# Optimization experiments

Hardware: AMD Instinct MI355X
Metric: run time of the kernel (lower is better)

Reference implementation:

```python
import jax, jax.numpy as jnp
import numpy as np

H_SPLITS = [2, 3, 3]          # crpe_window {3:2, 5:3, 7:3}
K_SIZES = [3, 5, 7]
NUM_HEADS = 8
EPS = 1e-6


def dwconv(x, w, b, k):
    # x: (B,C,H,W), w: (C,1,k,k) depthwise, 'same' padding
    y = jax.lax.conv_general_dilated(
        x, w, (1, 1), [(k // 2, k // 2)] * 2,
        feature_group_count=x.shape[1],
        dimension_numbers=('NCHW', 'OIHW', 'NCHW'))
    return y + b[None, :, None, None]


def layernorm(x, g, b):
    m = jnp.mean(x, -1, keepdims=True)
    v = jnp.var(x, -1, keepdims=True)
    return (x - m) * jax.lax.rsqrt(v + EPS) * g + b


def conv_rel_pos_enc(q, v, ws, bs, H, W):
    # ConvRelPosEnc (MPViT style, no cls token): q * depthwise_conv(v)
    B, h, N, Ch = q.shape
    v_img = v.transpose(0, 1, 3, 2).reshape(B, h * Ch, H, W)  # B (h Ch) H W
    splits = np.cumsum([hs * Ch for hs in H_SPLITS])[:-1]
    parts = jnp.split(v_img, splits, axis=1)
    conv_v = jnp.concatenate(
        [dwconv(p, w, b, k) for p, w, b, k in zip(parts, ws, bs, K_SIZES)], axis=1)
    conv_v = conv_v.reshape(B, h, Ch, N).transpose(0, 1, 3, 2)
    return q * conv_v


def setup_inputs() -> dict:
    key = jax.random.key(0)
    B, H, W, C, nd, r, mr = 8, 64, 64, 320, 4, 2, 4
    h = NUM_HEADS
    N = H * W
    Ch = C // h
    hid = C // r
    ks = jax.random.split(key, 16)
    s = 0.02
    return {
        'x': jax.random.normal(ks[0], (B, N, C), jnp.float32),
        'domain_label': jax.nn.one_hot(jax.random.randint(ks[1], (B,), 0, nd), nd, dtype=jnp.float32),
        'cpe_w': jax.random.normal(ks[2], (C, 1, 3, 3), jnp.float32) * s,
        'cpe_b': jnp.zeros((C,), jnp.float32),
        'ln1_g': jnp.ones((C,), jnp.float32), 'ln1_b': jnp.zeros((C,), jnp.float32),
        'qkv_w': jax.random.normal(ks[3], (3 * C, C), jnp.float32) * s,
        'qkv_b': jnp.zeros((3 * C,), jnp.float32),
        'crpe_w3': jax.random.normal(ks[4], (2 * Ch, 1, 3, 3), jnp.float32) * s,
        'crpe_b3': jnp.zeros((2 * Ch,), jnp.float32),
        'crpe_w5': jax.random.normal(ks[5], (3 * Ch, 1, 5, 5), jnp.float32) * s,
        'crpe_b5': jnp.zeros((3 * Ch,), jnp.float32),
        'crpe_w7': jax.random.normal(ks[6], (3 * Ch, 1, 7, 7), jnp.float32) * s,
        'crpe_b7': jnp.zeros((3 * Ch,), jnp.float32),
        'dom_w1': jax.random.normal(ks[7], (hid, nd), jnp.float32) * s,
        'dom_b1': jnp.zeros((hid,), jnp.float32),
        'dom_w2': jax.random.normal(ks[8], (C, hid), jnp.float32) * s,
        'dom_b2': jnp.zeros((C,), jnp.float32),
        'proj_w': jax.random.normal(ks[9], (C, C), jnp.float32) * s,
        'proj_b': jnp.zeros((C,), jnp.float32),
        'ln2_g': jnp.ones((C,), jnp.float32), 'ln2_b': jnp.zeros((C,), jnp.float32),
        'mlp_w1': jax.random.normal(ks[10], (mr * C, C), jnp.float32) * s,
        'mlp_b1': jnp.zeros((mr * C,), jnp.float32),
        'mlp_w2': jax.random.normal(ks[11], (C, mr * C), jnp.float32) * s,
        'mlp_b2': jnp.zeros((C,), jnp.float32),
        'H': H, 'W': W,
    }


def reference(x, domain_label, cpe_w, cpe_b, ln1_g, ln1_b, qkv_w, qkv_b,
              crpe_w3, crpe_b3, crpe_w5, crpe_b5, crpe_w7, crpe_b7,
              dom_w1, dom_b1, dom_w2, dom_b2, proj_w, proj_b,
              ln2_g, ln2_b, mlp_w1, mlp_b1, mlp_w2, mlp_b2, H, W):
    B, N, C = x.shape
    h = NUM_HEADS
    Ch = C // h
    scale = Ch ** -0.5
    # ConvPosEnc: depthwise 3x3 conv + residual
    img = x.transpose(0, 2, 1).reshape(B, C, H, W)
    x = (dwconv(img, cpe_w, cpe_b, 3) + img).reshape(B, C, N).transpose(0, 2, 1)
    # FactorAtt_ConvRelPosEnc_Sup
    cur = layernorm(x, ln1_g, ln1_b)
    qkv = (cur @ qkv_w.T + qkv_b).reshape(B, N, 3, h, Ch).transpose(2, 0, 3, 1, 4)
    q, k, v = qkv[0], qkv[1], qkv[2]          # (B,h,N,Ch) each
    k_sm = jax.nn.softmax(k, axis=2)          # softmax over tokens
    kv = jnp.einsum('bhnk,bhnv->bhkv', k_sm, v)   # (B,h,Ch,Ch)
    fa = jnp.einsum('bhnk,bhkv->bhnv', q, kv)
    fa = scale * fa + conv_rel_pos_enc(
        q, v, (crpe_w3, crpe_w5, crpe_w7), (crpe_b3, crpe_b5, crpe_b7), H, W)
    # domain gate: MLP(one_hot) -> softmax over heads, broadcast over tokens
    d = jax.nn.relu(domain_label @ dom_w1.T + dom_b1) @ dom_w2.T + dom_b2  # (B,C)
    d = jax.nn.softmax(d.reshape(B, h, 1, Ch), axis=1)
    att = (d * fa).transpose(0, 2, 1, 3).reshape(B, N, C)
    x = x + (att @ proj_w.T + proj_b)
    # MLP (GELU, ratio 4)
    cur = layernorm(x, ln2_g, ln2_b)
    cur = jax.nn.gelu(cur @ mlp_w1.T + mlp_b1, approximate=False) @ mlp_w2.T + mlp_b2
    return x + cur
```

## Files before the change

### kernel.cpp

```cpp
#include <hip/hip_runtime.h>
#include <hip/hip_bf16.h>
#include <math.h>
#include <type_traits>

#define B_    8
#define Nn    4096
#define Cc    320
#define QS    1024
#define ATT_SCALE 0.15811388300841897f

typedef __attribute__((ext_vector_type(8))) short s8v;
typedef __attribute__((ext_vector_type(4))) float f4v;

__device__ __forceinline__ float bf2f(short u) {
    return __uint_as_float(((unsigned int)(unsigned short)u) << 16);
}
__device__ __forceinline__ short f2bf(float f) {
    return (short)__bfloat16_as_ushort(__float2bfloat16(f));
}
__device__ __forceinline__ float gelu_fast(float v) {
    float u = v * (0.7978845608f + 0.0356774081f * v * v);
    float e = __expf(2.f * u);
    float t = 1.f - 2.f / (e + 1.f);
    return 0.5f * v * (1.f + t);
}

typedef const __attribute__((address_space(1))) unsigned int* gp1_t;
typedef __attribute__((address_space(3))) unsigned int* lp3_t;
__device__ __forceinline__ void gload16(const void* g, void* l) {
    __builtin_amdgcn_global_load_lds((gp1_t)g, (lp3_t)l, 16, 0, 0);
}

__global__ void cvt_all(const float* __restrict__ s0, const float* __restrict__ s1,
                        const float* __restrict__ s2, const float* __restrict__ s3,
                        __hip_bfloat16* __restrict__ d) {
    int i = blockIdx.x * 256 + threadIdx.x;
    if (i >= 1351680) return;
    const float* s; int j, rows, K;
    if (i < 327680)      { s = s0; j = i;          rows = 960;  K = 320; }
    else if (i < 450560) { s = s1; j = i - 327680; rows = 320;  K = 320; }
    else if (i < 860160) { s = s2; j = i - 450560; rows = 1280; K = 320; }
    else                 { s = s3; j = i - 860160; rows = 320;  K = 1280; }
    float v = (j / K < rows) ? s[j] : 0.f;
    d[i] = __float2bfloat16(v);
}

template<typename T>
__global__ void ln_kernel(const T* __restrict__ x, const float* __restrict__ g,
                          const float* __restrict__ bt, __hip_bfloat16* __restrict__ out) {
    int bn = blockIdx.x;
    int lane = threadIdx.x;
    const T* row = x + (size_t)bn * Cc;
    float v[5];
    float s = 0.f, s2 = 0.f;
    #pragma unroll
    for (int i = 0; i < 5; ++i) {
        if constexpr (std::is_same<T, float>::value) v[i] = row[lane + 64 * i];
        else v[i] = bf2f(((const short*)row)[lane + 64 * i]);
        s += v[i];
        s2 += v[i] * v[i];
    }
    #pragma unroll
    for (int off = 32; off > 0; off >>= 1) {
        s  += __shfl_down(s, off);
        s2 += __shfl_down(s2, off);
    }
    s  = __shfl(s, 0);
    s2 = __shfl(s2, 0);
    float mean = s * (1.f / 320.f);
    float var  = s2 * (1.f / 320.f) - mean * mean;
    float rstd = rsqrtf(var + 1e-6f);
    __hip_bfloat16* orow = out + (size_t)bn * Cc;
    #pragma unroll
    for (int i = 0; i < 5; ++i) {
        int c = lane + 64 * i;
        orow[c] = __float2bfloat16((v[i] - mean) * rstd * g[c] + bt[c]);
    }
}

template<int ACT, int RES, int WF32, int WBF16, int KT>
__global__ __launch_bounds__(512) void gemm_mfma(
        const __hip_bfloat16* __restrict__ A, const __hip_bfloat16* __restrict__ W,
        const float* __restrict__ bias, const void* __restrict__ resv,
        float* __restrict__ outf, __hip_bfloat16* __restrict__ outb,
        int NS, int Nreal, int gy) {
    __shared__ __align__(16) short As[256 * 64];
    __shared__ __align__(16) short Bs[128 * 64];
    int bid = blockIdx.x;
    int grp8 = gy << 3;
    int grp = bid / grp8, rem = bid % grp8;
    int m0 = ((grp << 3) + (rem & 7)) << 8;
    int n0 = (rem >> 3) << 7;
    int tid = threadIdx.x;
    int w = tid >> 6, lane = tid & 63;
    int wr = w >> 1, wc = w & 1;
    int lrow = lane & 15, lk = lane >> 4;
    f4v acc[4][4];
    #pragma unroll
    for (int i = 0; i < 4; ++i)
        #pragma unroll
        for (int j = 0; j < 4; ++j) acc[i][j] = (f4v){0.f, 0.f, 0.f, 0.f};

    int srow = (w << 3) + (lane >> 3);
    int slot = lane & 7;

    #pragma unroll
    for (int k0 = 0; k0 < KT; k0 += 64) {
        __syncthreads();
        #pragma unroll
        for (int i = 0; i < 4; ++i) {
            int row = i * 64 + srow;
            int sk = (slot ^ (row & 7)) << 3;
            gload16(&A[(size_t)(m0 + row) * KT + k0 + sk], &As[i * 4096 + w * 512]);
        }
        #pragma unroll
        for (int i = 0; i < 2; ++i) {
            int row = i * 64 + srow;
            int sk = (slot ^ (row & 7)) << 3;
            gload16(&W[(size_t)(n0 + row) * KT + k0 + sk], &Bs[i * 4096 + w * 512]);
        }
        __syncthreads();
        #pragma unroll
        for (int ks = 0; ks < 2; ++ks) {
            s8v af[4], bf[4];
            #pragma unroll
            for (int mi = 0; mi < 4; ++mi) {
                int row = wr * 64 + mi * 16 + lrow;
                int s = (ks * 4 + lk) ^ (row & 7);
                af[mi] = *reinterpret_cast<const s8v*>(&As[row * 64 + s * 8]);
            }
            #pragma unroll
            for (int ni = 0; ni < 4; ++ni) {
                int row = wc * 64 + ni * 16 + lrow;
                int s = (ks * 4 + lk) ^ (row & 7);
                bf[ni] = *reinterpret_cast<const s8v*>(&Bs[row * 64 + s * 8]);
            }
            #pragma unroll
            for (int mi = 0; mi < 4; ++mi)
                #pragma unroll
                for (int ni = 0; ni < 4; ++ni)
                    acc[mi][ni] = __builtin_amdgcn_mfma_f32_16x16x32_bf16(bf[ni], af[mi], acc[mi][ni], 0, 0, 0);
        }
    }
    #pragma unroll
    for (int mi = 0; mi < 4; ++mi) {
        int m = m0 + wr * 64 + mi * 16 + lrow;
        #pragma unroll
        for (int ni = 0; ni < 4; ++ni) {
            int n = n0 + wc * 64 + ni * 16 + (lk << 2);
            if (n >= Nreal) continue;
            f4v v4 = acc[mi][ni];
            float4 bv = *reinterpret_cast<const float4*>(&bias[n]);
            v4[0] += bv.x; v4[1] += bv.y; v4[2] += bv.z; v4[3] += bv.w;
            if (RES == 1) {
                const float* res = (const float*)resv;
                float4 rv = *reinterpret_cast<const float4*>(&res[(size_t)m * NS + n]);
                v4[0] += rv.x; v4[1] += rv.y; v4[2] += rv.z; v4[3] += rv.w;
            } else if (RES == 2) {
                const short* res = (const short*)resv;
                short4 rv = *reinterpret_cast<const short4*>(&res[(size_t)m * NS + n]);
                v4[0] += bf2f(rv.x); v4[1] += bf2f(rv.y);
                v4[2] += bf2f(rv.z); v4[3] += bf2f(rv.w);
            }
            if (ACT == 1) {
                #pragma unroll
                for (int r = 0; r < 4; ++r) v4[r] = gelu_fast(v4[r]);
            }
            if (WF32)
                *reinterpret_cast<float4*>(&outf[(size_t)m * NS + n]) =
                    make_float4(v4[0], v4[1], v4[2], v4[3]);
            if (WBF16) {
                ushort4 u;
                u.x = (unsigned short)f2bf(v4[0]);
                u.y = (unsigned short)f2bf(v4[1]);
                u.z = (unsigned short)f2bf(v4[2]);
                u.w = (unsigned short)f2bf(v4[3]);
                *reinterpret_cast<ushort4*>(&outb[(size_t)m * NS + n]) = u;
            }
        }
    }
}

template<int ACT, int RES, int WF32, int WBF16, int KT, int LN>
__global__ __launch_bounds__(512) void gemm_fulln(
        const __hip_bfloat16* __restrict__ A, const __hip_bfloat16* __restrict__ W,
        const float* __restrict__ bias, const void* __restrict__ resv,
        float* __restrict__ outf, __hip_bfloat16* __restrict__ outb, int NS,
        const float* __restrict__ lng, const float* __restrict__ lnb,
        __hip_bfloat16* __restrict__ lnout) {
    __shared__ __align__(16) short As[64 * 64];
    __shared__ __align__(16) short Ws[320 * 64];
    int tid = threadIdx.x;
    int m0 = blockIdx.x << 6;
    int w = tid >> 6, lane = tid & 63;
    int wr = w >> 2, wc = w & 3;
    int lrow = lane & 15, lk = lane >> 4;
    f4v acc[2][5];
    #pragma unroll
    for (int i = 0; i < 2; ++i)
        #pragma unroll
        for (int j = 0; j < 5; ++j) acc[i][j] = (f4v){0.f, 0.f, 0.f, 0.f};

    int srow = tid >> 3;
    int slot = tid & 7;

    #pragma unroll
    for (int k0 = 0; k0 < KT; k0 += 64) {
        __syncthreads();
        {
            int sk = (slot ^ (srow & 7)) << 3;
            gload16(&A[(size_t)(m0 + srow) * KT + k0 + sk], &As[w * 512]);
        }
        #pragma unroll
        for (int i = 0; i < 5; ++i) {
            int row = i * 64 + srow;
            int sk = (slot ^ (row & 7)) << 3;
            gload16(&W[(size_t)row * KT + k0 + sk], &Ws[i * 4096 + w * 512]);
        }
        __syncthreads();
        #pragma unroll
        for (int ks = 0; ks < 2; ++ks) {
            s8v af[2], bf[5];
            #pragma unroll
            for (int mi = 0; mi < 2; ++mi) {
                int row = wr * 32 + mi * 16 + lrow;
                int s = (ks * 4 + lk) ^ (row & 7);
                af[mi] = *reinterpret_cast<const s8v*>(&As[row * 64 + s * 8]);
            }
            #pragma unroll
            for (int ni = 0; ni < 5; ++ni) {
                int row = wc * 80 + ni * 16 + lrow;
                int s = (ks * 4 + lk) ^ (row & 7);
                bf[ni] = *reinterpret_cast<const s8v*>(&Ws[row * 64 + s * 8]);
            }
            #pragma unroll
            for (int mi = 0; mi < 2; ++mi)
                #pragma unroll
                for (int ni = 0; ni < 5; ++ni)
                    acc[mi][ni] = __builtin_amdgcn_mfma_f32_16x16x32_bf16(bf[ni], af[mi], acc[mi][ni], 0, 0, 0);
        }
    }
    float psum[2] = {0.f, 0.f}, psq[2] = {0.f, 0.f};
    #pragma unroll
    for (int mi = 0; mi < 2; ++mi) {
        int m = m0 + wr * 32 + mi * 16 + lrow;
        #pragma unroll
        for (int ni = 0; ni < 5; ++ni) {
            int n = wc * 80 + ni * 16 + (lk << 2);
            f4v v4 = acc[mi][ni];
            float4 bv = *reinterpret_cast<const float4*>(&bias[n]);
            v4[0] += bv.x; v4[1] += bv.y; v4[2] += bv.z; v4[3] += bv.w;
            if (RES == 1) {
                const float* res = (const float*)resv;
                float4 rv = *reinterpret_cast<const float4*>(&res[(size_t)m * NS + n]);
                v4[0] += rv.x; v4[1] += rv.y; v4[2] += rv.z; v4[3] += rv.w;
            } else if (RES == 2) {
                const short* res = (const short*)resv;
                short4 rv = *reinterpret_cast<const short4*>(&res[(size_t)m * NS + n]);
                v4[0] += bf2f(rv.x); v4[1] += bf2f(rv.y);
                v4[2] += bf2f(rv.z); v4[3] += bf2f(rv.w);
            }
            if (ACT == 1) {
                #pragma unroll
                for (int r = 0; r < 4; ++r) v4[r] = gelu_fast(v4[r]);
            }
            if (WF32)
                *reinterpret_cast<float4*>(&outf[(size_t)m * NS + n]) =
                    make_float4(v4[0], v4[1], v4[2], v4[3]);
            if (WBF16) {
                ushort4 u;
                u.x = (unsigned short)f2bf(v4[0]);
                u.y = (unsigned short)f2bf(v4[1]);
                u.z = (unsigned short)f2bf(v4[2]);
                u.w = (unsigned short)f2bf(v4[3]);
                *reinterpret_cast<ushort4*>(&outb[(size_t)m * NS + n]) = u;
            }
            if (LN) {
                acc[mi][ni] = v4;
                psum[mi] += v4[0] + v4[1] + v4[2] + v4[3];
                psq[mi]  += v4[0]*v4[0] + v4[1]*v4[1] + v4[2]*v4[2] + v4[3]*v4[3];
            }
        }
    }
    if (LN) {
        __syncthreads();
        float* red = (float*)As;
        #pragma unroll
        for (int mi = 0; mi < 2; ++mi) {
            int rl = wr * 32 + mi * 16 + lrow;
            red[(rl * 16 + wc * 4 + lk) * 2]     = psum[mi];
            red[(rl * 16 + wc * 4 + lk) * 2 + 1] = psq[mi];
        }
        __syncthreads();
        float* st = (float*)Ws;
        if (tid < 64) {
            float s = 0.f, q = 0.f;
            #pragma unroll
            for (int p = 0; p < 16; ++p) {
                s += red[(tid * 16 + p) * 2];
                q += red[(tid * 16 + p) * 2 + 1];
            }
            float mean = s * (1.f / 320.f);
            float var  = q * (1.f / 320.f) - mean * mean;
            st[tid * 2]     = mean;
            st[tid * 2 + 1] = rsqrtf(var + 1e-6f);
        }
        __syncthreads();
        #pragma unroll
        for (int mi = 0; mi < 2; ++mi) {
            int rl = wr * 32 + mi * 16 + lrow;
            int m = m0 + rl;
            float mean = st[rl * 2], rstd = st[rl * 2 + 1];
            #pragma unroll
            for (int ni = 0; ni < 5; ++ni) {
                int n = wc * 80 + ni * 16 + (lk << 2);
                float4 g4 = *reinterpret_cast<const float4*>(&lng[n]);
                float4 b4 = *reinterpret_cast<const float4*>(&lnb[n]);
                f4v v4 = acc[mi][ni];
                ushort4 u;
                u.x = (unsigned short)f2bf((v4[0] - mean) * rstd * g4.x + b4.x);
                u.y = (unsigned short)f2bf((v4[1] - mean) * rstd * g4.y + b4.y);
                u.z = (unsigned short)f2bf((v4[2] - mean) * rstd * g4.z + b4.z);
                u.w = (unsigned short)f2bf((v4[3] - mean) * rstd * g4.w + b4.w);
                *reinterpret_cast<ushort4*>(&lnout[(size_t)m * Cc + n]) = u;
            }
        }
    }
}

__global__ __launch_bounds__(256) void cpe_tile(
        const float* __restrict__ src, const float* __restrict__ wts,
        const float* __restrict__ bias, __hip_bfloat16* __restrict__ outb) {
    constexpr int P = 1, S = 18;
    __shared__ float vt[S * S * 8];
    __shared__ float ws_[8 * 9];
    int blk = blockIdx.x;
    int tile = blk & 15;
    int g  = (blk >> 4) % 40;
    int b  = (blk >> 4) / 40;
    int ty0 = (tile >> 2) << 4;
    int tx0 = (tile & 3) << 4;
    int c0 = g * 8;
    int tid = threadIdx.x;
    for (int e = tid; e < 72; e += 256) ws_[e] = wts[c0 * 9 + e];
    const float* sb = src + (size_t)b * Nn * Cc + c0;
    for (int e = tid; e < S * S; e += 256) {
        int hy = e / S, hx = e % S;
        int gy = ty0 - P + hy, gx = tx0 - P + hx;
        float px8[8];
        #pragma unroll
        for (int j = 0; j < 8; ++j) px8[j] = 0.f;
        if ((unsigned)gy < 64u && (unsigned)gx < 64u) {
            const float* p = &sb[(size_t)((gy << 6) + gx) * Cc];
            float4 lo = reinterpret_cast<const float4*>(p)[0];
            float4 hi = reinterpret_cast<const float4*>(p)[1];
            px8[0] = lo.x; px8[1] = lo.y; px8[2] = lo.z; px8[3] = lo.w;
            px8[4] = hi.x; px8[5] = hi.y; px8[6] = hi.z; px8[7] = hi.w;
        }
        #pragma unroll
        for (int j = 0; j < 8; ++j) vt[e * 8 + j] = px8[j];
    }
    __syncthreads();
    int cl  = tid & 7;
    int px  = (tid >> 3) & 15;
    int pyh = tid >> 7;
    int c = c0 + cl;
    float acc[8];
    float bval = bias[c];
    #pragma unroll
    for (int j = 0; j < 8; ++j) acc[j] = bval;
    #pragma unroll
    for (int dx = 0; dx < 3; ++dx) {
        float col[10];
        #pragma unroll
        for (int i = 0; i < 10; ++i)
            col[i] = vt[((pyh * 8 + i) * S + (px + dx)) * 8 + cl];
        #pragma unroll
        for (int j = 0; j < 8; ++j)
            #pragma unroll
            for (int dy = 0; dy < 3; ++dy)
                acc[j] += col[j + dy] * ws_[cl * 9 + dy * 3 + dx];
    }
    #pragma unroll
    for (int j = 0; j < 8; ++j) {
        int n = ((ty0 + pyh * 8 + j) << 6) + tx0 + px;
        size_t bn = (size_t)b * Nn + n;
        float ctr = vt[((pyh * 8 + j + P) * S + (px + P)) * 8 + cl];
        outb[bn * Cc + c] = __float2bfloat16(acc[j] + ctr);
    }
}

template<int KSZ>
__device__ __forceinline__ void crpe_body(
        float* vt, float* ws_, int tile, int b, int c0,
        const short* __restrict__ qkv, const float* __restrict__ wts,
        const float* __restrict__ bias,
        const short* __restrict__ fa0, const float* __restrict__ dg,
        short* __restrict__ outb) {
    constexpr int P = KSZ / 2;
    constexpr int S = 16 + 2 * P;
    int ty0 = (tile >> 2) << 4;
    int tx0 = (tile & 3) << 4;
    int tid = threadIdx.x;
    for (int e = tid; e < 8 * KSZ * KSZ; e += 256) ws_[e] = wts[e];
    const short* sb = qkv + (size_t)b * Nn * QS + 640 + c0;
    for (int e = tid; e < S * S; e += 256) {
        int hy = e / S, hx = e % S;
        int gy = ty0 - P + hy, gx = tx0 - P + hx;
        float px8[8];
        #pragma unroll
        for (int j = 0; j < 8; ++j) px8[j] = 0.f;
        if ((unsigned)gy < 64u && (unsigned)gx < 64u) {
            s8v v8 = *reinterpret_cast<const s8v*>(&sb[(size_t)((gy << 6) + gx) * QS]);
            #pragma unroll
            for (int j = 0; j < 8; ++j) px8[j] = bf2f(v8[j]);
        }
        #pragma unroll
        for (int j = 0; j < 8; ++j) vt[e * 8 + j] = px8[j];
    }
    __syncthreads();
    int cl  = tid & 7;
    int px  = (tid >> 3) & 15;
    int pyh = tid >> 7;
    int c = c0 + cl;
    float acc[8];
    float bval = bias[cl];
    #pragma unroll
    for (int j = 0; j < 8; ++j) acc[j] = bval;
    #pragma unroll
    for (int dx = 0; dx < KSZ; ++dx) {
        float col[8 + KSZ - 1];
        #pragma unroll
        for (int i = 0; i < 8 + KSZ - 1; ++i)
            col[i] = vt[((pyh * 8 + i) * S + (px + dx)) * 8 + cl];
        #pragma unroll
        for (int j = 0; j < 8; ++j)
            #pragma unroll
            for (int dy = 0; dy < KSZ; ++dy)
                acc[j] += col[j + dy] * ws_[cl * KSZ * KSZ + dy * KSZ + dx];
    }
    float dgv = dg[(size_t)b * Cc + c];
    #pragma unroll
    for (int j = 0; j < 8; ++j) {
        int n = ((ty0 + pyh * 8 + j) << 6) + tx0 + px;
        size_t bn = (size_t)b * Nn + n;
        float qv  = bf2f(qkv[bn * QS + c]);
        float fav = bf2f(fa0[bn * Cc + c]);
        float r = dgv * (ATT_SCALE * fav + qv * acc[j]);
        outb[bn * Cc + c] = __float2bfloat16(r);
    }
}

__global__ __launch_bounds__(256) void crpe_all(
        const __hip_bfloat16* __restrict__ qkv,
        const float* __restrict__ w3, const float* __restrict__ b3,
        const float* __restrict__ w5, const float* __restrict__ b5,
        const float* __restrict__ w7, const float* __restrict__ b7,
        const __hip_bfloat16* __restrict__ fa, const float* __restrict__ dg,
        __hip_bfloat16* __restrict__ outb) {
    __shared__ float vt[22 * 22 * 8];
    __shared__ float ws_[8 * 49];
    int blk = blockIdx.x;
    int tile = blk & 15;
    int g = (blk >> 4) % 40;
    int b = (blk >> 4) / 40;
    int c0 = g * 8;
    if (g < 10)
        crpe_body<3>(vt, ws_, tile, b, c0, (const short*)qkv,
                     w3 + c0 * 9, b3 + c0, (const short*)fa, dg, (short*)outb);
    else if (g < 25)
        crpe_body<5>(vt, ws_, tile, b, c0, (const short*)qkv,
                     w5 + (c0 - 80) * 25, b5 + (c0 - 80), (const short*)fa, dg, (short*)outb);
    else
        crpe_body<7>(vt, ws_, tile, b, c0, (const short*)qkv,
                     w7 + (c0 - 200) * 49, b7 + (c0 - 200), (const short*)fa, dg, (short*)outb);
}

__global__ __launch_bounds__(256) void kv_mfma(const __hip_bfloat16* __restrict__ qkv,
                                               float* __restrict__ kvp) {
    __shared__ short lds[4 * 2 * 48 * 66];
    int blk = blockIdx.x;
    int s = blk & 7;
    int bh = blk >> 3;
    int h = bh & 7, b = bh >> 3;
    int tid = threadIdx.x;
    int w = tid >> 6, lane = tid & 63;
    short* ke_t = lds + w * 2 * 48 * 66;
    short* vv_t = ke_t + 48 * 66;
    for (int e = lane; e < 8 * 66; e += 64) {
        ke_t[40 * 66 + e] = 0;
        vv_t[40 * 66 + e] = 0;
    }
    for (int n = lane; n < 66; n += 64) vv_t[40 * 66 + n] = (short)0x3F80;

    const short* kb = (const short*)qkv + (size_t)b * Nn * QS + 320 + h * 40;
    const short* vb = kb + 320;
    int col0 = lane & 15, kq = lane >> 4;
    f4v acc[3][3];
    #pragma unroll
    for (int i = 0; i < 3; ++i)
        #pragma unroll
        for (int j = 0; j < 3; ++j) acc[i][j] = (f4v){0.f, 0.f, 0.f, 0.f};

    for (int t = w; t < 8; t += 4) {
        int n0 = s * 512 + t * 64;
        for (int e = lane; e < 320; e += 64) {
            int nl = e / 5, oct = e % 5;
            size_t go = (size_t)(n0 + nl) * QS + oct * 8;
            s8v k8 = *reinterpret_cast<const s8v*>(kb + go);
            s8v v8 = *reinterpret_cast<const s8v*>(vb + go);
            #pragma unroll
            for (int j = 0; j < 8; ++j) {
                ke_t[(oct * 8 + j) * 66 + nl] = f2bf(__expf(bf2f(k8[j])));
                vv_t[(oct * 8 + j) * 66 + nl] = v8[j];
            }
        }
        __syncthreads();
        #pragma unroll
        for (int ks = 0; ks < 2; ++ks) {
            s8v af[3], bfr[3];
            #pragma unroll
            for (int mt = 0; mt < 3; ++mt)
                af[mt] = *reinterpret_cast<const s8v*>(ke_t + (mt * 16 + col0) * 66 + ks * 32 + kq * 8);
            #pragma unroll
            for (int nt = 0; nt < 3; ++nt)
                bfr[nt] = *reinterpret_cast<const s8v*>(vv_t + (nt * 16 + col0) * 66 + ks * 32 + kq * 8);
            #pragma unroll
            for (int mt = 0; mt < 3; ++mt)
                #pragma unroll
                for (int nt = 0; nt < 3; ++nt)
                    acc[mt][nt] = __builtin_amdgcn_mfma_f32_16x16x32_bf16(af[mt], bfr[nt], acc[mt][nt], 0, 0, 0);
        }
        __syncthreads();
    }
    float* red = (float*)lds;
    #pragma unroll
    for (int mt = 0; mt < 3; ++mt) {
        #pragma unroll
        for (int nt = 0; nt < 3; ++nt) {
            #pragma unroll
            for (int r = 0; r < 4; ++r) {
                int ch = mt * 16 + kq * 4 + r;
                int cv = nt * 16 + col0;
                if (ch < 40) red[w * 1920 + ch * 48 + cv] = acc[mt][nt][r];
            }
        }
    }
    __syncthreads();
    for (int p = tid; p < 1920; p += 256) {
        float sv = red[p] + red[1920 + p] + red[2 * 1920 + p] + red[3 * 1920 + p];
        kvp[(size_t)blk * 1920 + p] = sv;
    }
}

__global__ void kv_combine2(const float* __restrict__ kvp, float* __restrict__ kv) {
    int bh = blockIdx.x;
    int tid = threadIdx.x;
    __shared__ float sinv[40];
    if (tid < 40) {
        float S = 0.f;
        for (int s2 = 0; s2 < 8; ++s2)
            S += kvp[(size_t)(bh * 8 + s2) * 1920 + tid * 48 + 40];
        sinv[tid] = 1.f / S;
    }
    __syncthreads();
    for (int p = tid; p < 1600; p += 256) {
        int ch = p / 40, cv = p % 40;
        float v = 0.f;
        for (int s2 = 0; s2 < 8; ++s2)
            v += kvp[(size_t)(bh * 8 + s2) * 1920 + ch * 48 + cv];
        kv[(size_t)bh * 1600 + p] = v * sinv[ch];
    }
}

__global__ void dgate_kernel(const float* __restrict__ lbl, const float* __restrict__ w1,
                             const float* __restrict__ b1, const float* __restrict__ w2,
                             const float* __restrict__ b2, float* __restrict__ dg) {
    int b = blockIdx.x;
    int tid = threadIdx.x;
    __shared__ float hid[160];
    __shared__ float dd[320];
    if (tid < 160) {
        float a = b1[tid];
        for (int d = 0; d < 4; ++d) a += w1[tid * 4 + d] * lbl[b * 4 + d];
        hid[tid] = fmaxf(a, 0.f);
    }
    __syncthreads();
    float a = b2[tid];
    for (int j = 0; j < 160; ++j) a += w2[tid * 160 + j] * hid[j];
    dd[tid] = a;
    __syncthreads();
    if (tid < 40) {
        float M = -1e30f;
        for (int h2 = 0; h2 < 8; ++h2) M = fmaxf(M, dd[h2 * 40 + tid]);
        float S = 0.f;
        float e[8];
        for (int h2 = 0; h2 < 8; ++h2) { e[h2] = __expf(dd[h2 * 40 + tid] - M); S += e[h2]; }
        float inv = 1.f / S;
        for (int h2 = 0; h2 < 8; ++h2) dg[b * 320 + h2 * 40 + tid] = e[h2] * inv;
    }
}

__global__ __launch_bounds__(256) void fa_kernel(const __hip_bfloat16* __restrict__ qkv,
        const float* __restrict__ kvmat, __hip_bfloat16* __restrict__ fa) {
    __shared__ float kvs[1600];
    int blk = blockIdx.x;
    int chunk = blk & 15;
    int bh = blk >> 4;
    int h = bh & 7, b = bh >> 3;
    int tid = threadIdx.x;
    for (int e = tid; e < 1600; e += 256) kvs[e] = kvmat[(size_t)bh * 1600 + e];
    __syncthreads();
    int n = chunk * 256 + tid;
    const short* qr = (const short*)qkv + (size_t)(b * Nn + n) * QS + h * 40;
    float q[40];
    #pragma unroll
    for (int i = 0; i < 5; ++i) {
        s8v v8 = reinterpret_cast<const s8v*>(qr)[i];
        #pragma unroll
        for (int j = 0; j < 8; ++j) q[i * 8 + j] = bf2f(v8[j]);
    }
    float o[40];
    #pragma unroll
    for (int cv = 0; cv < 40; ++cv) o[cv] = 0.f;
    #pragma unroll
    for (int ch = 0; ch < 40; ++ch) {
        float qv = q[ch];
        #pragma unroll
        for (int cv = 0; cv < 40; ++cv)
            o[cv] += qv * kvs[ch * 40 + cv];
    }
    short* fr = (short*)fa + (size_t)(b * Nn + n) * 320 + h * 40;
    #pragma unroll
    for (int i = 0; i < 5; ++i) {
        s8v u;
        #pragma unroll
        for (int j = 0; j < 8; ++j) u[j] = f2bf(o[i * 8 + j]);
        *reinterpret_cast<s8v*>(fr + i * 8) = u;
    }
}

extern "C" void kernel_launch(void* const* d_in, const int* in_sizes, int n_in,
                              void* d_out, int out_size, void* d_ws, size_t ws_size,
                              hipStream_t stream) {
    const float* x     = (const float*)d_in[0];
    const float* lbl   = (const float*)d_in[1];
    const float* cpe_w = (const float*)d_in[2];
    const float* cpe_b = (const float*)d_in[3];
    const float* ln1g  = (const float*)d_in[4];
    const float* ln1b  = (const float*)d_in[5];
    const float* qkv_w = (const float*)d_in[6];
    const float* qkv_b = (const float*)d_in[7];
    const float* w3    = (const float*)d_in[8];
    const float* b3    = (const float*)d_in[9];
    const float* w5    = (const float*)d_in[10];
    const float* b5    = (const float*)d_in[11];
    const float* w7    = (const float*)d_in[12];
    const float* b7    = (const float*)d_in[13];
    const float* dw1   = (const float*)d_in[14];
    const float* db1   = (const float*)d_in[15];
    const float* dw2   = (const float*)d_in[16];
    const float* db2   = (const float*)d_in[17];
    const float* pw    = (const float*)d_in[18];
    const float* pb    = (const float*)d_in[19];
    const float* ln2g  = (const float*)d_in[20];
    const float* ln2b  = (const float*)d_in[21];
    const float* m1w   = (const float*)d_in[22];
    const float* m1b   = (const float*)d_in[23];
    const float* m2w   = (const float*)d_in[24];
    const float* m2b   = (const float*)d_in[25];
    float* out = (float*)d_out;

    float* ws = (float*)d_ws;
    __hip_bfloat16* x1b  = (__hip_bfloat16*)ws; ws += 5242880;
    __hip_bfloat16* qkvb = (__hip_bfloat16*)ws; ws += 16777216;
    float* big  = ws; ws += 20971520;
    __hip_bfloat16* gelub = (__hip_bfloat16*)big;
    __hip_bfloat16* fab   = (__hip_bfloat16*)ws; ws += 5242880;
    __hip_bfloat16* bb1   = (__hip_bfloat16*)ws; ws += 5242880;
    __hip_bfloat16* wb    = (__hip_bfloat16*)ws; ws += 675840;
    float* kvp  = ws; ws += 983040;
    float* kv   = ws; ws += 102400;
    float* dg   = ws; ws += 2560;
    __hip_bfloat16* wbq  = wb;
    __hip_bfloat16* wbp  = wbq  + 1024 * 320;
    __hip_bfloat16* wbm1 = wbp  + 384 * 320;
    __hip_bfloat16* wbm2 = wbm1 + 1280 * 320;

    cvt_all<<<5280, 256, 0, stream>>>(qkv_w, pw, m1w, m2w, wb);
    cpe_tile<<<B_ * 40 * 16, 256, 0, stream>>>(x, cpe_w, cpe_b, x1b);
    ln_kernel<__hip_bfloat16><<<B_ * Nn, 64, 0, stream>>>(x1b, ln1g, ln1b, bb1);
    gemm_mfma<0, 0, 0, 1, 320><<<1024, 512, 0, stream>>>(bb1, wbq, qkv_b, nullptr,
                                                         nullptr, qkvb, QS, 960, 8);
    kv_mfma<<<512, 256, 0, stream>>>(qkvb, kvp);
    kv_combine2<<<64, 256, 0, stream>>>(kvp, kv);
    dgate_kernel<<<B_, 320, 0, stream>>>(lbl, dw1, db1, dw2, db2, dg);
    fa_kernel<<<B_ * 8 * 16, 256, 0, stream>>>(qkvb, kv, fab);
    crpe_all<<<B_ * 40 * 16, 256, 0, stream>>>(qkvb, w3, b3, w5, b5, w7, b7,
                                               fab, dg, bb1);
    gemm_fulln<0, 2, 1, 0, 320, 1><<<512, 512, 0, stream>>>(bb1, wbp, pb, x1b,
                                                            out, nullptr, 320,
                                                            ln2g, ln2b, bb1);
    gemm_mfma<1, 0, 0, 1, 320><<<1280, 512, 0, stream>>>(bb1, wbm1, m1b, nullptr,
                                                         nullptr, gelub, 1280, 1280, 10);
    gemm_fulln<0, 1, 1, 0, 1280, 0><<<512, 512, 0, stream>>>(gelub, wbm2, m2b, out,
                                                             out, nullptr, 320,
                                                             nullptr, nullptr, nullptr);
}
```

Before: 299.7 us.

## Fuse factor-attention matmul into CRPE kernel and halve M-tile for MLP2 GEMM

Removes the standalone fa_kernel and its bf16 intermediate buffer. The q@kv product is now computed inside crpe_all: each block stages its tile's q rows and the needed kv slice in LDS, and each thread computes the fa value for its own channel. This drops a full write and read of an intermediate tensor, but every block recomputes a 40-length dot product per output and uses more LDS, which can lower occupancy. The fulln GEMM also gains an M-tile template parameter, and the final MLP down-projection uses 32-row tiles with twice as many blocks for better parallelism.

```diff
diff --git a/kernel.cpp b/kernel.cpp
--- a/kernel.cpp
+++ b/kernel.cpp
@@ -181,23 +181,24 @@
     }
 }
 
-template<int ACT, int RES, int WF32, int WBF16, int KT, int LN>
+template<int ACT, int RES, int WF32, int WBF16, int KT, int LN, int MT>
 __global__ __launch_bounds__(512) void gemm_fulln(
         const __hip_bfloat16* __restrict__ A, const __hip_bfloat16* __restrict__ W,
         const float* __restrict__ bias, const void* __restrict__ resv,
         float* __restrict__ outf, __hip_bfloat16* __restrict__ outb, int NS,
         const float* __restrict__ lng, const float* __restrict__ lnb,
         __hip_bfloat16* __restrict__ lnout) {
-    __shared__ __align__(16) short As[64 * 64];
+    constexpr int MI = MT / 32;
+    __shared__ __align__(16) short As[MT * 64];
     __shared__ __align__(16) short Ws[320 * 64];
     int tid = threadIdx.x;
-    int m0 = blockIdx.x << 6;
+    int m0 = blockIdx.x * MT;
     int w = tid >> 6, lane = tid & 63;
     int wr = w >> 2, wc = w & 3;
     int lrow = lane & 15, lk = lane >> 4;
-    f4v acc[2][5];
-    #pragma unroll
-    for (int i = 0; i < 2; ++i)
+    f4v acc[MI][5];
+    #pragma unroll
+    for (int i = 0; i < MI; ++i)
         #pragma unroll
         for (int j = 0; j < 5; ++j) acc[i][j] = (f4v){0.f, 0.f, 0.f, 0.f};
 
@@ -207,7 +208,7 @@
     #pragma unroll
     for (int k0 = 0; k0 < KT; k0 += 64) {
         __syncthreads();
-        {
+        if (MT == 64 || w < 4) {
             int sk = (slot ^ (srow & 7)) << 3;
             gload16(&A[(size_t)(m0 + srow) * KT + k0 + sk], &As[w * 512]);
         }
@@ -220,10 +221,10 @@
         __syncthreads();
         #pragma unroll
         for (int ks = 0; ks < 2; ++ks) {
-            s8v af[2], bf[5];
-            #pragma unroll
-            for (int mi = 0; mi < 2; ++mi) {
-                int row = wr * 32 + mi * 16 + lrow;
+            s8v af[MI], bf[5];
+            #pragma unroll
+            for (int mi = 0; mi < MI; ++mi) {
+                int row = (MT == 64 ? wr * 32 + mi * 16 : wr * 16) + lrow;
                 int s = (ks * 4 + lk) ^ (row & 7);
                 af[mi] = *reinterpret_cast<const s8v*>(&As[row * 64 + s * 8]);
             }
@@ -234,16 +235,19 @@
                 bf[ni] = *reinterpret_cast<const s8v*>(&Ws[row * 64 + s * 8]);
             }
             #pragma unroll
-            for (int mi = 0; mi < 2; ++mi)
+            for (int mi = 0; mi < MI; ++mi)
                 #pragma unroll
                 for (int ni = 0; ni < 5; ++ni)
                     acc[mi][ni] = __builtin_amdgcn_mfma_f32_16x16x32_bf16(bf[ni], af[mi], acc[mi][ni], 0, 0, 0);
         }
     }
-    float psum[2] = {0.f, 0.f}, psq[2] = {0.f, 0.f};
-    #pragma unroll
-    for (int mi = 0; mi < 2; ++mi) {
-        int m = m0 + wr * 32 + mi * 16 + lrow;
+    float psum[MI], psq[MI];
+    #pragma unroll
+    for (int i = 0; i < MI; ++i) { psum[i] = 0.f; psq[i] = 0.f; }
+    #pragma unroll
+    for (int mi = 0; mi < MI; ++mi) {
+        int rl = (MT == 64 ? wr * 32 + mi * 16 : wr * 16) + lrow;
+        int m = m0 + rl;
         #pragma unroll
         for (int ni = 0; ni < 5; ++ni) {
             int n = wc * 80 + ni * 16 + (lk << 2);
@@ -286,7 +290,7 @@
         __syncthreads();
         float* red = (float*)As;
         #pragma unroll
-        for (int mi = 0; mi < 2; ++mi) {
+        for (int mi = 0; mi < MI; ++mi) {
             int rl = wr * 32 + mi * 16 + lrow;
             red[(rl * 16 + wc * 4 + lk) * 2]     = psum[mi];
             red[(rl * 16 + wc * 4 + lk) * 2 + 1] = psq[mi];
@@ -307,7 +311,7 @@
         }
         __syncthreads();
         #pragma unroll
-        for (int mi = 0; mi < 2; ++mi) {
+        for (int mi = 0; mi < MI; ++mi) {
             int rl = wr * 32 + mi * 16 + lrow;
             int m = m0 + rl;
             float mean = st[rl * 2], rstd = st[rl * 2 + 1];
@@ -392,17 +396,31 @@
 
 template<int KSZ>
 __device__ __forceinline__ void crpe_body(
-        float* vt, float* ws_, int tile, int b, int c0,
+        float* vt, float* ws_, short* q_lds, float* kvsl,
+        int tile, int b, int c0,
         const short* __restrict__ qkv, const float* __restrict__ wts,
-        const float* __restrict__ bias,
-        const short* __restrict__ fa0, const float* __restrict__ dg,
-        short* __restrict__ outb) {
+        const float* __restrict__ bias, const float* __restrict__ kvmat,
+        const float* __restrict__ dg, short* __restrict__ outb) {
     constexpr int P = KSZ / 2;
     constexpr int S = 16 + 2 * P;
     int ty0 = (tile >> 2) << 4;
     int tx0 = (tile & 3) << 4;
     int tid = threadIdx.x;
+    int h   = c0 / 40;
+    int cv0 = c0 % 40;
+    int bh  = b * 8 + h;
     for (int e = tid; e < 8 * KSZ * KSZ; e += 256) ws_[e] = wts[e];
+    {
+        int y = tid >> 4, xg = tid & 15;
+        int n = ((ty0 + y) << 6) + tx0 + xg;
+        const short* qr = qkv + ((size_t)b * Nn + n) * QS + h * 40;
+        #pragma unroll
+        for (int i = 0; i < 5; ++i)
+            *reinterpret_cast<s8v*>(&q_lds[tid * 40 + i * 8]) =
+                reinterpret_cast<const s8v*>(qr)[i];
+    }
+    for (int e = tid; e < 320; e += 256)
+        kvsl[e] = kvmat[(size_t)bh * 1600 + (e >> 3) * 40 + cv0 + (e & 7)];
     const short* sb = qkv + (size_t)b * Nn * QS + 640 + c0;
     for (int e = tid; e < S * S; e += 256) {
         int hy = e / S, hx = e % S;
@@ -439,14 +457,29 @@
             for (int dy = 0; dy < KSZ; ++dy)
                 acc[j] += col[j + dy] * ws_[cl * KSZ * KSZ + dy * KSZ + dx];
     }
+    float kvr[40];
+    #pragma unroll
+    for (int ch = 0; ch < 40; ++ch) kvr[ch] = kvsl[ch * 8 + cl];
     float dgv = dg[(size_t)b * Cc + c];
     #pragma unroll
     for (int j = 0; j < 8; ++j) {
-        int n = ((ty0 + pyh * 8 + j) << 6) + tx0 + px;
+        int py = pyh * 8 + j;
+        int p  = py * 16 + px;
+        float fa = 0.f;
+        float qv = 0.f;
+        #pragma unroll
+        for (int i = 0; i < 5; ++i) {
+            s8v q8 = *reinterpret_cast<const s8v*>(&q_lds[p * 40 + i * 8]);
+            #pragma unroll
+            for (int t = 0; t < 8; ++t) {
+                float qf = bf2f(q8[t]);
+                fa += qf * kvr[i * 8 + t];
+                if (i * 8 + t == cv0 + cl) qv = qf;
+            }
+        }
+        int n = (py + ty0) * 64 + tx0 + px;
         size_t bn = (size_t)b * Nn + n;
-        float qv  = bf2f(qkv[bn * QS + c]);
-        float fav = bf2f(fa0[bn * Cc + c]);
-        float r = dgv * (ATT_SCALE * fav + qv * acc[j]);
+        float r = dgv * (ATT_SCALE * fa + qv * acc[j]);
         outb[bn * Cc + c] = __float2bfloat16(r);
     }
 }
@@ -456,24 +489,26 @@
         const float* __restrict__ w3, const float* __restrict__ b3,
         const float* __restrict__ w5, const float* __restrict__ b5,
         const float* __restrict__ w7, const float* __restrict__ b7,
-        const __hip_bfloat16* __restrict__ fa, const float* __restrict__ dg,
+        const float* __restrict__ kvmat, const float* __restrict__ dg,
         __hip_bfloat16* __restrict__ outb) {
     __shared__ float vt[22 * 22 * 8];
     __shared__ float ws_[8 * 49];
+    __shared__ short q_lds[256 * 40];
+    __shared__ float kvsl[320];
     int blk = blockIdx.x;
     int tile = blk & 15;
     int g = (blk >> 4) % 40;
     int b = (blk >> 4) / 40;
     int c0 = g * 8;
     if (g < 10)
-        crpe_body<3>(vt, ws_, tile, b, c0, (const short*)qkv,
-                     w3 + c0 * 9, b3 + c0, (const short*)fa, dg, (short*)outb);
+        crpe_body<3>(vt, ws_, q_lds, kvsl, tile, b, c0, (const short*)qkv,
+                     w3 + c0 * 9, b3 + c0, kvmat, dg, (short*)outb);
     else if (g < 25)
-        crpe_body<5>(vt, ws_, tile, b, c0, (const short*)qkv,
-                     w5 + (c0 - 80) * 25, b5 + (c0 - 80), (const short*)fa, dg, (short*)outb);
+        crpe_body<5>(vt, ws_, q_lds, kvsl, tile, b, c0, (const short*)qkv,
+                     w5 + (c0 - 80) * 25, b5 + (c0 - 80), kvmat, dg, (short*)outb);
     else
-        crpe_body<7>(vt, ws_, tile, b, c0, (const short*)qkv,
-                     w7 + (c0 - 200) * 49, b7 + (c0 - 200), (const short*)fa, dg, (short*)outb);
+        crpe_body<7>(vt, ws_, q_lds, kvsl, tile, b, c0, (const short*)qkv,
+                     w7 + (c0 - 200) * 49, b7 + (c0 - 200), kvmat, dg, (short*)outb);
 }
 
 __global__ __launch_bounds__(256) void kv_mfma(const __hip_bfloat16* __restrict__ qkv,
@@ -598,45 +633,6 @@
         for (int h2 = 0; h2 < 8; ++h2) { e[h2] = __expf(dd[h2 * 40 + tid] - M); S += e[h2]; }
         float inv = 1.f / S;
         for (int h2 = 0; h2 < 8; ++h2) dg[b * 320 + h2 * 40 + tid] = e[h2] * inv;
-    }
-}
-
-__global__ __launch_bounds__(256) void fa_kernel(const __hip_bfloat16* __restrict__ qkv,
-        const float* __restrict__ kvmat, __hip_bfloat16* __restrict__ fa) {
-    __shared__ float kvs[1600];
-    int blk = blockIdx.x;
-    int chunk = blk & 15;
-    int bh = blk >> 4;
-    int h = bh & 7, b = bh >> 3;
-    int tid = threadIdx.x;
-    for (int e = tid; e < 1600; e += 256) kvs[e] = kvmat[(size_t)bh * 1600 + e];
-    __syncthreads();
-    int n = chunk * 256 + tid;
-    const short* qr = (const short*)qkv + (size_t)(b * Nn + n) * QS + h * 40;
-    float q[40];
-    #pragma unroll
-    for (int i = 0; i < 5; ++i) {
-        s8v v8 = reinterpret_cast<const s8v*>(qr)[i];
-        #pragma unroll
-        for (int j = 0; j < 8; ++j) q[i * 8 + j] = bf2f(v8[j]);
-    }
-    float o[40];
-    #pragma unroll
-    for (int cv = 0; cv < 40; ++cv) o[cv] = 0.f;
-    #pragma unroll
-    for (int ch = 0; ch < 40; ++ch) {
-        float qv = q[ch];
-        #pragma unroll
-        for (int cv = 0; cv < 40; ++cv)
-            o[cv] += qv * kvs[ch * 40 + cv];
-    }
-    short* fr = (short*)fa + (size_t)(b * Nn + n) * 320 + h * 40;
-    #pragma unroll
-    for (int i = 0; i < 5; ++i) {
-        s8v u;
-        #pragma unroll
-        for (int j = 0; j < 8; ++j) u[j] = f2bf(o[i * 8 + j]);
-        *reinterpret_cast<s8v*>(fr + i * 8) = u;
     }
 }
 
@@ -676,7 +672,6 @@
     __hip_bfloat16* qkvb = (__hip_bfloat16*)ws; ws += 16777216;
     float* big  = ws; ws += 20971520;
     __hip_bfloat16* gelub = (__hip_bfloat16*)big;
-    __hip_bfloat16* fab   = (__hip_bfloat16*)ws; ws += 5242880;
     __hip_bfloat16* bb1   = (__hip_bfloat16*)ws; ws += 5242880;
     __hip_bfloat16* wb    = (__hip_bfloat16*)ws; ws += 675840;
     float* kvp  = ws; ws += 983040;
@@ -695,15 +690,14 @@
     kv_mfma<<<512, 256, 0, stream>>>(qkvb, kvp);
     kv_combine2<<<64, 256, 0, stream>>>(kvp, kv);
     dgate_kernel<<<B_, 320, 0, stream>>>(lbl, dw1, db1, dw2, db2, dg);
-    fa_kernel<<<B_ * 8 * 16, 256, 0, stream>>>(qkvb, kv, fab);
     crpe_all<<<B_ * 40 * 16, 256, 0, stream>>>(qkvb, w3, b3, w5, b5, w7, b7,
-                                               fab, dg, bb1);
-    gemm_fulln<0, 2, 1, 0, 320, 1><<<512, 512, 0, stream>>>(bb1, wbp, pb, x1b,
-                                                            out, nullptr, 320,
-                                                            ln2g, ln2b, bb1);
+                                               kv, dg, bb1);
+    gemm_fulln<0, 2, 1, 0, 320, 1, 64><<<512, 512, 0, stream>>>(bb1, wbp, pb, x1b,
+                                                                out, nullptr, 320,
+                                                                ln2g, ln2b, bb1);
     gemm_mfma<1, 0, 0, 1, 320><<<1280, 512, 0, stream>>>(bb1, wbm1, m1b, nullptr,
                                                          nullptr, gelub, 1280, 1280, 10);
-    gemm_fulln<0, 1, 1, 0, 1280, 0><<<512, 512, 0, stream>>>(gelub, wbm2, m2b, out,
-                                                             out, nullptr, 320,
-                                                             nullptr, nullptr, nullptr);
-}
+    gemm_fulln<0, 1, 1, 0, 1280, 0, 32><<<1024, 512, 0, stream>>>(gelub, wbm2, m2b, out,
+                                                                  out, nullptr, 320,
+                                                                  nullptr, nullptr, nullptr);
+}
```

Measured after the change: 318.1 us. +6.1%, slower.

## Double-buffer GEMM LDS tiles with K-step 32 to overlap loads and MFMA

Applied to the files above, without the earlier changes.

Restructures the generic MFMA GEMM main loop to use two LDS buffers with a K-chunk of 32 instead of a single 64-wide buffer. The next chunk's global-to-LDS loads are issued before computing the current one, with explicit vmcnt waits and raw s_barriers replacing the two __syncthreads per step. The aim is to hide global load latency behind MFMA work, at the cost of more loop iterations, more barriers and a 4-way swizzle that may raise LDS bank conflicts.

```diff
diff --git a/kernel.cpp b/kernel.cpp
--- a/kernel.cpp
+++ b/kernel.cpp
@@ -84,8 +84,9 @@
         const float* __restrict__ bias, const void* __restrict__ resv,
         float* __restrict__ outf, __hip_bfloat16* __restrict__ outb,
         int NS, int Nreal, int gy) {
-    __shared__ __align__(16) short As[256 * 64];
-    __shared__ __align__(16) short Bs[128 * 64];
+    constexpr int NSTEP = KT / 32;
+    __shared__ __align__(16) short As[2][256 * 32];
+    __shared__ __align__(16) short Bs[2][128 * 32];
     int bid = blockIdx.x;
     int grp8 = gy << 3;
     int grp = bid / grp8, rem = bid % grp8;
@@ -101,46 +102,52 @@
         #pragma unroll
         for (int j = 0; j < 4; ++j) acc[i][j] = (f4v){0.f, 0.f, 0.f, 0.f};
 
-    int srow = (w << 3) + (lane >> 3);
-    int slot = lane & 7;
-
-    #pragma unroll
-    for (int k0 = 0; k0 < KT; k0 += 64) {
-        __syncthreads();
-        #pragma unroll
-        for (int i = 0; i < 4; ++i) {
-            int row = i * 64 + srow;
-            int sk = (slot ^ (row & 7)) << 3;
-            gload16(&A[(size_t)(m0 + row) * KT + k0 + sk], &As[i * 4096 + w * 512]);
-        }
+    int ua0 = (w << 6) + lane;
+    auto STAGE = [&](int buf, int k0) {
         #pragma unroll
         for (int i = 0; i < 2; ++i) {
-            int row = i * 64 + srow;
-            int sk = (slot ^ (row & 7)) << 3;
-            gload16(&W[(size_t)(n0 + row) * KT + k0 + sk], &Bs[i * 4096 + w * 512]);
-        }
-        __syncthreads();
-        #pragma unroll
-        for (int ks = 0; ks < 2; ++ks) {
-            s8v af[4], bf[4];
-            #pragma unroll
-            for (int mi = 0; mi < 4; ++mi) {
-                int row = wr * 64 + mi * 16 + lrow;
-                int s = (ks * 4 + lk) ^ (row & 7);
-                af[mi] = *reinterpret_cast<const s8v*>(&As[row * 64 + s * 8]);
-            }
-            #pragma unroll
-            for (int ni = 0; ni < 4; ++ni) {
-                int row = wc * 64 + ni * 16 + lrow;
-                int s = (ks * 4 + lk) ^ (row & 7);
-                bf[ni] = *reinterpret_cast<const s8v*>(&Bs[row * 64 + s * 8]);
-            }
-            #pragma unroll
-            for (int mi = 0; mi < 4; ++mi)
-                #pragma unroll
-                for (int ni = 0; ni < 4; ++ni)
-                    acc[mi][ni] = __builtin_amdgcn_mfma_f32_16x16x32_bf16(bf[ni], af[mi], acc[mi][ni], 0, 0, 0);
-        }
+            int u = ua0 + i * 512;
+            int row = u >> 2, slot = u & 3;
+            int sk = (slot ^ (row & 3)) << 3;
+            gload16(&A[(size_t)(m0 + row) * KT + k0 + sk], &As[buf][i * 4096 + w * 512]);
+        }
+        {
+            int u = ua0;
+            int row = u >> 2, slot = u & 3;
+            int sk = (slot ^ (row & 3)) << 3;
+            gload16(&W[(size_t)(n0 + row) * KT + k0 + sk], &Bs[buf][w * 512]);
+        }
+    };
+
+    STAGE(0, 0);
+    #pragma unroll
+    for (int step = 0; step < NSTEP; ++step) {
+        int buf = step & 1;
+        if (step + 1 < NSTEP) {
+            STAGE(buf ^ 1, (step + 1) * 32);
+            asm volatile("s_waitcnt vmcnt(3)" ::: "memory");
+        } else {
+            asm volatile("s_waitcnt vmcnt(0)" ::: "memory");
+        }
+        __builtin_amdgcn_sched_barrier(0);
+        __builtin_amdgcn_s_barrier();
+        s8v af[4], bf[4];
+        #pragma unroll
+        for (int mi = 0; mi < 4; ++mi) {
+            int row = wr * 64 + mi * 16 + lrow;
+            af[mi] = *reinterpret_cast<const s8v*>(&As[buf][row * 32 + ((lk ^ (row & 3)) << 3)]);
+        }
+        #pragma unroll
+        for (int ni = 0; ni < 4; ++ni) {
+            int row = wc * 64 + ni * 16 + lrow;
+            bf[ni] = *reinterpret_cast<const s8v*>(&Bs[buf][row * 32 + ((lk ^ (row & 3)) << 3)]);
+        }
+        #pragma unroll
+        for (int mi = 0; mi < 4; ++mi)
+            #pragma unroll
+            for (int ni = 0; ni < 4; ++ni)
+                acc[mi][ni] = __builtin_amdgcn_mfma_f32_16x16x32_bf16(bf[ni], af[mi], acc[mi][ni], 0, 0, 0);
+        __builtin_amdgcn_s_barrier();
     }
     #pragma unroll
     for (int mi = 0; mi < 4; ++mi) {
@@ -243,7 +250,8 @@
     float psum[2] = {0.f, 0.f}, psq[2] = {0.f, 0.f};
     #pragma unroll
     for (int mi = 0; mi < 2; ++mi) {
-        int m = m0 + wr * 32 + mi * 16 + lrow;
+        int rl = wr * 32 + mi * 16 + lrow;
+        int m = m0 + rl;
         #pragma unroll
         for (int ni = 0; ni < 5; ++ni) {
             int n = wc * 80 + ni * 16 + (lk << 2);
```

New measurement: 299.2 us. No clear change (-0.2%).
